# Optimization experiments

Measured on AMD Instinct MI355X. Metric: run time of the kernel, lower is better.

Reference implementation:

```python
import jax, jax.numpy as jnp
import numpy as np

EPS_OT = 0.1        # args.model.ot_reg
N_ITERS = 5         # args.model.ot_transport
COS_EPS = 1e-8      # torch F.cosine_similarity eps
L2_EPS = 1e-12      # torch F.normalize eps
LN_EPS = 1e-5       # nn.LayerNorm default eps
IN_DIM, HID = 768, 256


def setup_inputs() -> dict:
    key = jax.random.key(0)
    ks = jax.random.split(key, 8)
    Ba, Bb, Sa, Sb = 48, 48, 96, 96
    s_in = 1.0 / np.sqrt(IN_DIM)
    return {
        "batch_a": jax.random.normal(ks[0], (Ba, Sa, IN_DIM), jnp.float32),
        "batch_b": jax.random.normal(ks[1], (Bb, Sb, IN_DIM), jnp.float32),
        "Wq": jax.random.normal(ks[2], (IN_DIM, HID), jnp.float32) * s_in,
        "bq": jnp.zeros((HID,), jnp.float32),
        "Wk": jax.random.normal(ks[3], (IN_DIM, HID), jnp.float32) * s_in,
        "bk": jnp.zeros((HID,), jnp.float32),
        "Wv": jax.random.normal(ks[4], (IN_DIM, HID), jnp.float32) * s_in,
        "bv": jnp.zeros((HID,), jnp.float32),
        "ln_g": jnp.ones((HID,), jnp.float32),
        "ln_b": jnp.zeros((HID,), jnp.float32),
    }


def _layernorm(x, g, b):
    mu = jnp.mean(x, axis=-1, keepdims=True)
    var = jnp.var(x, axis=-1, keepdims=True)
    return (x - mu) * jax.lax.rsqrt(var + LN_EPS) * g + b


def _sinkhorn(C):
    # multiplicative Sinkhorn on kernel exp(C/eps); row/col renormalization
    T = jnp.exp(C / EPS_OT)  # [Ba,Bb,Sa,Sb]
    def body(_, T):
        T = T / jnp.sum(T, axis=-1, keepdims=True)
        T = T / jnp.sum(T, axis=-2, keepdims=True)
        return T
    return jax.lax.fori_loop(0, N_ITERS, body, T)


def reference(batch_a, batch_b, Wq, bq, Wk, bk, Wv, bv, ln_g, ln_b):
    q = batch_a @ Wq + bq          # [Ba,Sa,H]
    k = batch_b @ Wk + bk          # [Bb,Sb,H]
    v = batch_b @ Wv + bv          # [Bb,Sb,H]

    # cosine similarity across batches: [Ba,Bb,Sa,Sb]
    qn = q / jnp.maximum(jnp.linalg.norm(q, axis=-1, keepdims=True), COS_EPS)
    kn = k / jnp.maximum(jnp.linalg.norm(k, axis=-1, keepdims=True), COS_EPS)
    C = jnp.einsum('aid,bjd->abij', qn, kn)

    T = jax.lax.stop_gradient(_sinkhorn(C))  # C.detach() in source
    # F.normalize(dim=-1): L2 over last dim
    T = T / jnp.maximum(jnp.linalg.norm(T, axis=-1, keepdims=True), L2_EPS)
    # dropout p=0.0 -> identity (eval)

    attended = jnp.einsum('abij,bjd->abid', T, v) + q[:, None]  # [Ba,Bb,Sa,H]
    return _layernorm(attended, ln_g, ln_b)
```

## Files before the change

### kernel.cpp

```cpp
#include <hip/hip_runtime.h>
#include <hip/hip_bf16.h>

typedef __attribute__((ext_vector_type(4))) float f32x4;
typedef __attribute__((ext_vector_type(8))) short bf16x8;
typedef __attribute__((ext_vector_type(4))) short s16x4;

#define BA 48
#define BB 48
#define SS 96
#define DIN 768
#define HH 256

static __device__ __forceinline__ short f2bf(float f) {
    __hip_bfloat16 h = __float2bfloat16(f);
    return *reinterpret_cast<short*>(&h);
}

static __device__ __forceinline__ f32x4 mfma16(bf16x8 a, bf16x8 b, f32x4 c) {
    return __builtin_amdgcn_mfma_f32_16x16x32_bf16(a, b, c, 0, 0, 0);
}

__global__ __launch_bounds__(256) void prep_kernel(
    const float* __restrict__ Xa, const float* __restrict__ Xb,
    const float* __restrict__ Wq, const float* __restrict__ Wk,
    const float* __restrict__ Wv,
    short* __restrict__ xa, short* __restrict__ xb, short* __restrict__ wt) {
    __shared__ float tile[64][65];
    int bx = blockIdx.x;
    if (bx < 3456) {
        size_t i = (size_t)bx * 256 + threadIdx.x;
        const float* src;
        short* dst;
        size_t off;
        if (i < 442368) { src = Xa; dst = xa; off = i * 8; }
        else            { src = Xb; dst = xb; off = (i - 442368) * 8; }
        f32x4 a = *reinterpret_cast<const f32x4*>(src + off);
        f32x4 b = *reinterpret_cast<const f32x4*>(src + off + 4);
        bf16x8 o;
        o[0] = f2bf(a[0]); o[1] = f2bf(a[1]); o[2] = f2bf(a[2]); o[3] = f2bf(a[3]);
        o[4] = f2bf(b[0]); o[5] = f2bf(b[1]); o[6] = f2bf(b[2]); o[7] = f2bf(b[3]);
        *reinterpret_cast<bf16x8*>(dst + off) = o;
    } else {
        int tt = bx - 3456;
        int k0 = (tt % 12) * 64;
        int n0 = ((tt / 12) % 4) * 64;
        int mat = tt / 48;
        const float* W = (mat == 0) ? Wq : (mat == 1) ? Wk : Wv;
        int t = threadIdx.x;
#pragma unroll
        for (int j = 0; j < 16; ++j) {
            int kk = j * 4 + (t >> 6);
            int nn = t & 63;
            tile[kk][nn] = W[(size_t)(k0 + kk) * HH + n0 + nn];
        }
        __syncthreads();
#pragma unroll
        for (int j = 0; j < 4; ++j) {
            int nn = j * 16 + (t >> 4);
            int kk = (t & 15) * 4;
            s16x4 pk;
#pragma unroll
            for (int i = 0; i < 4; ++i) pk[i] = f2bf(tile[kk + i][nn]);
            *reinterpret_cast<s16x4*>(&wt[(size_t)(mat * HH + n0 + nn) * DIN + k0 + kk]) = pk;
        }
    }
}

__global__ __launch_bounds__(384) void qkv_kernel(
    const short* __restrict__ xa, const short* __restrict__ xb,
    const float* __restrict__ bq, const float* __restrict__ bk, const float* __restrict__ bv,
    const short* __restrict__ wt,
    float* __restrict__ q_ws, float* __restrict__ k_ws, short* __restrict__ vt_ws) {
    __shared__ short vtile[32][104];

    int bb = blockIdx.x;
    int mat = blockIdx.y;
    int c0 = blockIdx.z * 32;
    int tid = threadIdx.x;
    int wave = tid >> 6, lane = tid & 63;
    int c = lane & 15, g = lane >> 4;

    const short* X = ((mat == 0) ? xa : xb) + (size_t)bb * SS * DIN;
    const short* Wt = wt + (size_t)mat * HH * DIN;
    const float* bias = (mat == 0) ? bq : (mat == 1) ? bk : bv;

    const f32x4 z4 = {0.f, 0.f, 0.f, 0.f};
    f32x4 acc[2];
    acc[0] = z4; acc[1] = z4;

    const short* ap = X + (16 * wave + c) * DIN + g * 8;
    const short* bp = Wt + (c0 + c) * DIN + g * 8;
    for (int kk = 0; kk < DIN; kk += 32) {
        bf16x8 af = *reinterpret_cast<const bf16x8*>(ap + kk);
#pragma unroll
        for (int n = 0; n < 2; ++n) {
            bf16x8 bf = *reinterpret_cast<const bf16x8*>(bp + n * 16 * DIN + kk);
            acc[n] = mfma16(af, bf, acc[n]);
        }
    }
#pragma unroll
    for (int n = 0; n < 2; ++n) {
        float bv_ = bias[c0 + n * 16 + c];
#pragma unroll
        for (int r = 0; r < 4; ++r) acc[n][r] += bv_;
    }

    if (mat < 2) {
        float* dst = (mat == 0) ? q_ws : k_ws;
#pragma unroll
        for (int n = 0; n < 2; ++n)
#pragma unroll
            for (int r = 0; r < 4; ++r)
                dst[(bb * SS + 16 * wave + 4 * g + r) * HH + c0 + n * 16 + c] = acc[n][r];
    } else {
#pragma unroll
        for (int n = 0; n < 2; ++n)
#pragma unroll
            for (int r = 0; r < 4; ++r)
                vtile[n * 16 + c][16 * wave + 4 * g + r] = f2bf(acc[n][r]);
        __syncthreads();
        {
            int t = tid;
            int d = t / 12, ch = t % 12;
            bf16x8 pk = *reinterpret_cast<const bf16x8*>(&vtile[d][ch * 8]);
            *reinterpret_cast<bf16x8*>(vt_ws + ((size_t)(bb * HH) + c0 + d) * SS + ch * 8) = pk;
        }
    }
}

__global__ __launch_bounds__(256) void norm_kernel(
    const float* __restrict__ q_ws, const float* __restrict__ k_ws,
    short* __restrict__ qn_ws, short* __restrict__ kn_ws) {
    int row = blockIdx.x * 4 + (threadIdx.x >> 6);
    int lane = threadIdx.x & 63;
    int isq = (row < 4608);
    const float* src = isq ? q_ws : k_ws;
    short* dst = isq ? qn_ws : kn_ws;
    int r = isq ? row : row - 4608;

    f32x4 v = *reinterpret_cast<const f32x4*>(src + (size_t)r * HH + lane * 4);
    float s = v[0] * v[0] + v[1] * v[1] + v[2] * v[2] + v[3] * v[3];
#pragma unroll
    for (int m = 1; m < 64; m <<= 1) s += __shfl_xor(s, m);
    float inv = 1.0f / fmaxf(sqrtf(s), 1e-8f);
    s16x4 o;
#pragma unroll
    for (int j = 0; j < 4; ++j) o[j] = f2bf(v[j] * inv);
    *reinterpret_cast<s16x4*>(dst + (size_t)r * HH + lane * 4) = o;
}

__global__ __launch_bounds__(256, 2) void sink_kernel(
    const short* __restrict__ qn_ws, const short* __restrict__ kn_ws,
    short* __restrict__ t_ws, int a_off) {
    int wave = threadIdx.x >> 6, lane = threadIdx.x & 63;
    int c = lane & 15, g = lane >> 4;
    int b = blockIdx.x * 4 + wave;
    int al = blockIdx.y;
    int a = al + a_off;

    const short* qbase = qn_ws + (size_t)(a * SS) * HH + c * HH + g * 8;
    const short* kbase = kn_ws + (size_t)(b * SS) * HH + c * HH + g * 8;

    const f32x4 z4 = {0.f, 0.f, 0.f, 0.f};
    f32x4 K[6][6];
#pragma unroll
    for (int ti = 0; ti < 6; ++ti)
#pragma unroll
        for (int tj = 0; tj < 6; ++tj) K[ti][tj] = z4;

#pragma unroll
    for (int kk = 0; kk < 8; ++kk) {
        bf16x8 qf[6];
#pragma unroll
        for (int ti = 0; ti < 6; ++ti)
            qf[ti] = *reinterpret_cast<const bf16x8*>(qbase + ti * 16 * HH + kk * 32);
#pragma unroll
        for (int tj = 0; tj < 6; ++tj) {
            bf16x8 kf = *reinterpret_cast<const bf16x8*>(kbase + tj * 16 * HH + kk * 32);
#pragma unroll
            for (int ti = 0; ti < 6; ++ti)
                K[ti][tj] = mfma16(kf, qf[ti], K[ti][tj]);
        }
    }

#pragma unroll
    for (int ti = 0; ti < 6; ++ti)
#pragma unroll
        for (int tj = 0; tj < 6; ++tj)
#pragma unroll
            for (int r = 0; r < 4; ++r)
                K[ti][tj][r] = exp2f(K[ti][tj][r] * 14.4269504088896341f);

    f32x4 v[6];
#pragma unroll
    for (int tj = 0; tj < 6; ++tj) v[tj] = (f32x4){1.f, 1.f, 1.f, 1.f};
    float u[6];

#pragma unroll 1
    for (int it = 0; it < 5; ++it) {
#pragma unroll
        for (int ti = 0; ti < 6; ++ti) {
            f32x4 p0 = K[ti][0] * v[0] + K[ti][1] * v[1];
            f32x4 p1 = K[ti][2] * v[2] + K[ti][3] * v[3];
            f32x4 p2 = K[ti][4] * v[4] + K[ti][5] * v[5];
            f32x4 p = (p0 + p1) + p2;
            float rs = (p[0] + p[1]) + (p[2] + p[3]);
            rs += __shfl_xor(rs, 16);
            rs += __shfl_xor(rs, 32);
            u[ti] = 1.0f / rs;
        }
#pragma unroll
        for (int tj = 0; tj < 6; ++tj) {
            f32x4 c0 = K[0][tj] * u[0] + K[1][tj] * u[1];
            f32x4 c1 = K[2][tj] * u[2] + K[3][tj] * u[3];
            f32x4 c2 = K[4][tj] * u[4] + K[5][tj] * u[5];
            f32x4 cs = (c0 + c1) + c2;
#pragma unroll
            for (int m = 1; m < 16; m <<= 1)
#pragma unroll
                for (int r = 0; r < 4; ++r) cs[r] += __shfl_xor(cs[r], m);
#pragma unroll
            for (int r = 0; r < 4; ++r) v[tj][r] = 1.0f / cs[r];
        }
    }

    short* tp = t_ws + (size_t)(al * BB + b) * SS * SS;
#pragma unroll
    for (int ti = 0; ti < 6; ++ti) {
        f32x4 w[6];
#pragma unroll
        for (int tj = 0; tj < 6; ++tj) w[tj] = K[ti][tj] * v[tj];
        f32x4 q0 = w[0] * w[0] + w[1] * w[1];
        f32x4 q1 = w[2] * w[2] + w[3] * w[3];
        f32x4 q2 = w[4] * w[4] + w[5] * w[5];
        f32x4 qq = (q0 + q1) + q2;
        float ss = (qq[0] + qq[1]) + (qq[2] + qq[3]);
        ss += __shfl_xor(ss, 16);
        ss += __shfl_xor(ss, 32);
        float linv = 1.0f / fmaxf(sqrtf(ss), 1e-12f);
#pragma unroll
        for (int tj = 0; tj < 6; ++tj) {
            s16x4 pk;
#pragma unroll
            for (int r = 0; r < 4; ++r) pk[r] = f2bf(w[tj][r] * linv);
            *reinterpret_cast<s16x4*>(tp + (16 * ti + c) * SS + 16 * tj + 4 * g) = pk;
        }
    }
}

__global__ __launch_bounds__(512) void pv_kernel(
    const short* __restrict__ t_ws, const short* __restrict__ vt_ws,
    const float* __restrict__ q_ws,
    const float* __restrict__ ln_g, const float* __restrict__ ln_b,
    float* __restrict__ out, int a_off) {
    __shared__ float wstats[8][2][SS];

    int b = blockIdx.x, al = blockIdx.y;
    int a = al + a_off;
    int tid = threadIdx.x;
    int w = tid >> 6, lane = tid & 63;
    int c = lane & 15, g = lane >> 4;
    int d0 = w * 32;

    const f32x4 z4 = {0.f, 0.f, 0.f, 0.f};
    f32x4 acc[2][6];
#pragma unroll
    for (int dt = 0; dt < 2; ++dt)
#pragma unroll
        for (int ti = 0; ti < 6; ++ti) acc[dt][ti] = z4;

    const short* vp = vt_ws + ((size_t)(b * HH) + d0 + c) * SS + g * 8;
    const short* tp = t_ws + ((size_t)(al * BB + b)) * SS * SS + c * SS + g * 8;
#pragma unroll
    for (int ks = 0; ks < 3; ++ks) {
        bf16x8 af0 = *reinterpret_cast<const bf16x8*>(vp + ks * 32);
        bf16x8 af1 = *reinterpret_cast<const bf16x8*>(vp + 16 * SS + ks * 32);
#pragma unroll
        for (int ti = 0; ti < 6; ++ti) {
            bf16x8 bf = *reinterpret_cast<const bf16x8*>(tp + ti * 16 * SS + ks * 32);
            acc[0][ti] = mfma16(af0, bf, acc[0][ti]);
            acc[1][ti] = mfma16(af1, bf, acc[1][ti]);
        }
    }

    const float* qa = q_ws + (size_t)a * SS * HH;
#pragma unroll
    for (int ti = 0; ti < 6; ++ti) {
        int i = 16 * ti + c;
        f32x4 q0 = *reinterpret_cast<const f32x4*>(qa + (size_t)i * HH + d0 + 4 * g);
        f32x4 q1 = *reinterpret_cast<const f32x4*>(qa + (size_t)i * HH + d0 + 16 + 4 * g);
        f32x4 x0 = acc[0][ti] + q0;
        f32x4 x1 = acc[1][ti] + q1;
        acc[0][ti] = x0;
        acc[1][ti] = x1;
        f32x4 sv = x0 + x1;
        f32x4 qv = x0 * x0 + x1 * x1;
        float l1 = (sv[0] + sv[1]) + (sv[2] + sv[3]);
        float l2 = (qv[0] + qv[1]) + (qv[2] + qv[3]);
        l1 += __shfl_xor(l1, 16);
        l1 += __shfl_xor(l1, 32);
        l2 += __shfl_xor(l2, 16);
        l2 += __shfl_xor(l2, 32);
        if (g == 0) {
            wstats[w][0][i] = l1;
            wstats[w][1][i] = l2;
        }
    }
    __syncthreads();

    f32x4 g4[2], b4[2];
#pragma unroll
    for (int dt = 0; dt < 2; ++dt) {
        g4[dt] = *reinterpret_cast<const f32x4*>(ln_g + d0 + dt * 16 + 4 * g);
        b4[dt] = *reinterpret_cast<const f32x4*>(ln_b + d0 + dt * 16 + 4 * g);
    }

    float* ob = out + ((size_t)(a * BB + b)) * SS * HH;
#pragma unroll
    for (int ti = 0; ti < 6; ++ti) {
        int i = 16 * ti + c;
        float t1 = ((wstats[0][0][i] + wstats[1][0][i]) + (wstats[2][0][i] + wstats[3][0][i])) +
                   ((wstats[4][0][i] + wstats[5][0][i]) + (wstats[6][0][i] + wstats[7][0][i]));
        float t2 = ((wstats[0][1][i] + wstats[1][1][i]) + (wstats[2][1][i] + wstats[3][1][i])) +
                   ((wstats[4][1][i] + wstats[5][1][i]) + (wstats[6][1][i] + wstats[7][1][i]));
        float mean = t1 * (1.0f / 256.0f);
        float var = t2 * (1.0f / 256.0f) - mean * mean;
        float inv = rsqrtf(var + 1e-5f);
#pragma unroll
        for (int dt = 0; dt < 2; ++dt) {
            f32x4 x = acc[dt][ti];
            f32x4 o;
#pragma unroll
            for (int r = 0; r < 4; ++r)
                o[r] = (x[r] - mean) * inv * g4[dt][r] + b4[dt][r];
            *reinterpret_cast<f32x4*>(ob + (size_t)i * HH + d0 + dt * 16 + 4 * g) = o;
        }
    }
}

extern "C" void kernel_launch(void* const* d_in, const int* in_sizes, int n_in,
                              void* d_out, int out_size, void* d_ws, size_t ws_size,
                              hipStream_t stream) {
    const float* Xa = (const float*)d_in[0];
    const float* Xb = (const float*)d_in[1];
    const float* Wq = (const float*)d_in[2];
    const float* bq = (const float*)d_in[3];
    const float* Wk = (const float*)d_in[4];
    const float* bk = (const float*)d_in[5];
    const float* Wv = (const float*)d_in[6];
    const float* bv = (const float*)d_in[7];
    const float* ln_g = (const float*)d_in[8];
    const float* ln_b = (const float*)d_in[9];
    float* out = (float*)d_out;

    char* ws = (char*)d_ws;
    short* wt    = (short*)(ws);
    short* xa_bf = (short*)(ws + 1179648);
    short* xb_bf = (short*)(ws + 8257536);
    float* q_ws  = (float*)(ws + 15335424);
    float* k_ws  = (float*)(ws + 20054016);
    short* qn_ws = (short*)(ws + 24772608);
    short* kn_ws = (short*)(ws + 27131904);
    short* vt_ws = (short*)(ws + 29491200);

    const size_t t_full = (size_t)BA * BB * SS * SS * 2;
    size_t t_off = 31850496;
    size_t avail = (ws_size > t_off) ? ws_size - t_off : 0;
    int nch;
    if (avail >= t_full) nch = 1;
    else if (avail >= t_full / 2) nch = 2;
    else if (avail >= t_full / 4) nch = 4;
    else { nch = 4; t_off = 0; }
    short* t_ws = (short*)(ws + t_off);
    int apc = BA / nch;

    prep_kernel<<<dim3(3600), dim3(256), 0, stream>>>(Xa, Xb, Wq, Wk, Wv,
                                                      xa_bf, xb_bf, wt);
    qkv_kernel<<<dim3(BA, 3, 8), dim3(384), 0, stream>>>(xa_bf, xb_bf, bq, bk, bv, wt,
                                                         q_ws, k_ws, vt_ws);
    norm_kernel<<<dim3(2304), dim3(256), 0, stream>>>(q_ws, k_ws, qn_ws, kn_ws);
    for (int ch = 0; ch < nch; ++ch) {
        sink_kernel<<<dim3(12, apc), dim3(256), 0, stream>>>(qn_ws, kn_ws, t_ws, ch * apc);
        pv_kernel<<<dim3(BB, apc), dim3(512), 0, stream>>>(t_ws, vt_ws, q_ws,
                                                           ln_g, ln_b, out, ch * apc);
    }
}
```

Baseline: 238.3 us.

## Fuse L2 row normalization into QKV projection kernel, drop norm kernel

Q and K projection blocks now compute all 256 output columns per row, so each block can apply the bias and do the row L2 normalization in registers and write bf16 qn/kn directly. The separate norm kernel, its launch, and the fp32 k_ws round trip are removed. V projection keeps the old 32-column split. The trade-off is far fewer, heavier Q/K blocks (96 instead of 768) that each hold 16 accumulators, which lowers parallelism in that stage and uses uncoalesced scalar stores.

```diff
diff --git a/kernel.cpp b/kernel.cpp
--- a/kernel.cpp
+++ b/kernel.cpp
@@ -66,53 +66,98 @@
     }
 }
 
-__global__ __launch_bounds__(384) void qkv_kernel(
+__global__ __launch_bounds__(384) void qkvn_kernel(
     const short* __restrict__ xa, const short* __restrict__ xb,
     const float* __restrict__ bq, const float* __restrict__ bk, const float* __restrict__ bv,
     const short* __restrict__ wt,
-    float* __restrict__ q_ws, float* __restrict__ k_ws, short* __restrict__ vt_ws) {
+    float* __restrict__ q_ws, short* __restrict__ qn_ws,
+    short* __restrict__ kn_ws, short* __restrict__ vt_ws) {
     __shared__ short vtile[32][104];
 
     int bb = blockIdx.x;
-    int mat = blockIdx.y;
-    int c0 = blockIdx.z * 32;
+    int y = blockIdx.y;
     int tid = threadIdx.x;
     int wave = tid >> 6, lane = tid & 63;
     int c = lane & 15, g = lane >> 4;
 
-    const short* X = ((mat == 0) ? xa : xb) + (size_t)bb * SS * DIN;
-    const short* Wt = wt + (size_t)mat * HH * DIN;
-    const float* bias = (mat == 0) ? bq : (mat == 1) ? bk : bv;
-
     const f32x4 z4 = {0.f, 0.f, 0.f, 0.f};
-    f32x4 acc[2];
-    acc[0] = z4; acc[1] = z4;
-
-    const short* ap = X + (16 * wave + c) * DIN + g * 8;
-    const short* bp = Wt + (c0 + c) * DIN + g * 8;
-    for (int kk = 0; kk < DIN; kk += 32) {
-        bf16x8 af = *reinterpret_cast<const bf16x8*>(ap + kk);
+
+    if (y < 2) {
+        int mat = y;
+        const short* X = ((mat == 0) ? xa : xb) + (size_t)bb * SS * DIN;
+        const short* Wt = wt + (size_t)mat * HH * DIN;
+        const float* bias = (mat == 0) ? bq : bk;
+
+        f32x4 acc[16];
+#pragma unroll
+        for (int n = 0; n < 16; ++n) acc[n] = z4;
+
+        const short* ap = X + (16 * wave + c) * DIN + g * 8;
+        const short* bp = Wt + c * DIN + g * 8;
+        for (int kk = 0; kk < DIN; kk += 32) {
+            bf16x8 af = *reinterpret_cast<const bf16x8*>(ap + kk);
+#pragma unroll
+            for (int n = 0; n < 16; ++n) {
+                bf16x8 bf = *reinterpret_cast<const bf16x8*>(bp + n * 16 * DIN + kk);
+                acc[n] = mfma16(af, bf, acc[n]);
+            }
+        }
+#pragma unroll
+        for (int n = 0; n < 16; ++n) {
+            float bv_ = bias[n * 16 + c];
+#pragma unroll
+            for (int r = 0; r < 4; ++r) acc[n][r] += bv_;
+        }
+
+        float s2[4] = {0.f, 0.f, 0.f, 0.f};
+#pragma unroll
+        for (int n = 0; n < 16; ++n)
+#pragma unroll
+            for (int r = 0; r < 4; ++r) s2[r] += acc[n][r] * acc[n][r];
+#pragma unroll
+        for (int m = 1; m < 16; m <<= 1)
+#pragma unroll
+            for (int r = 0; r < 4; ++r) s2[r] += __shfl_xor(s2[r], m);
+        float inv[4];
+#pragma unroll
+        for (int r = 0; r < 4; ++r) inv[r] = 1.0f / fmaxf(sqrtf(s2[r]), 1e-8f);
+
+        short* qn = (mat == 0) ? qn_ws : kn_ws;
+#pragma unroll
+        for (int n = 0; n < 16; ++n) {
+#pragma unroll
+            for (int r = 0; r < 4; ++r) {
+                int row = bb * SS + 16 * wave + 4 * g + r;
+                int col = n * 16 + c;
+                if (mat == 0) q_ws[(size_t)row * HH + col] = acc[n][r];
+                qn[(size_t)row * HH + col] = f2bf(acc[n][r] * inv[r]);
+            }
+        }
+    } else {
+        int c0 = (y - 2) * 32;
+        const short* X = xb + (size_t)bb * SS * DIN;
+        const short* Wt = wt + (size_t)2 * HH * DIN;
+
+        f32x4 acc[2];
+        acc[0] = z4; acc[1] = z4;
+
+        const short* ap = X + (16 * wave + c) * DIN + g * 8;
+        const short* bp = Wt + (c0 + c) * DIN + g * 8;
+        for (int kk = 0; kk < DIN; kk += 32) {
+            bf16x8 af = *reinterpret_cast<const bf16x8*>(ap + kk);
+#pragma unroll
+            for (int n = 0; n < 2; ++n) {
+                bf16x8 bf = *reinterpret_cast<const bf16x8*>(bp + n * 16 * DIN + kk);
+                acc[n] = mfma16(af, bf, acc[n]);
+            }
+        }
 #pragma unroll
         for (int n = 0; n < 2; ++n) {
-            bf16x8 bf = *reinterpret_cast<const bf16x8*>(bp + n * 16 * DIN + kk);
-            acc[n] = mfma16(af, bf, acc[n]);
-        }
-    }
-#pragma unroll
-    for (int n = 0; n < 2; ++n) {
-        float bv_ = bias[c0 + n * 16 + c];
-#pragma unroll
-        for (int r = 0; r < 4; ++r) acc[n][r] += bv_;
-    }
-
-    if (mat < 2) {
-        float* dst = (mat == 0) ? q_ws : k_ws;
-#pragma unroll
-        for (int n = 0; n < 2; ++n)
-#pragma unroll
-            for (int r = 0; r < 4; ++r)
-                dst[(bb * SS + 16 * wave + 4 * g + r) * HH + c0 + n * 16 + c] = acc[n][r];
-    } else {
+            float bv_ = bv[c0 + n * 16 + c];
+#pragma unroll
+            for (int r = 0; r < 4; ++r) acc[n][r] += bv_;
+        }
+
 #pragma unroll
         for (int n = 0; n < 2; ++n)
 #pragma unroll
@@ -126,27 +171,6 @@
             *reinterpret_cast<bf16x8*>(vt_ws + ((size_t)(bb * HH) + c0 + d) * SS + ch * 8) = pk;
         }
     }
-}
-
-__global__ __launch_bounds__(256) void norm_kernel(
-    const float* __restrict__ q_ws, const float* __restrict__ k_ws,
-    short* __restrict__ qn_ws, short* __restrict__ kn_ws) {
-    int row = blockIdx.x * 4 + (threadIdx.x >> 6);
-    int lane = threadIdx.x & 63;
-    int isq = (row < 4608);
-    const float* src = isq ? q_ws : k_ws;
-    short* dst = isq ? qn_ws : kn_ws;
-    int r = isq ? row : row - 4608;
-
-    f32x4 v = *reinterpret_cast<const f32x4*>(src + (size_t)r * HH + lane * 4);
-    float s = v[0] * v[0] + v[1] * v[1] + v[2] * v[2] + v[3] * v[3];
-#pragma unroll
-    for (int m = 1; m < 64; m <<= 1) s += __shfl_xor(s, m);
-    float inv = 1.0f / fmaxf(sqrtf(s), 1e-8f);
-    s16x4 o;
-#pragma unroll
-    for (int j = 0; j < 4; ++j) o[j] = f2bf(v[j] * inv);
-    *reinterpret_cast<s16x4*>(dst + (size_t)r * HH + lane * 4) = o;
 }
 
 __global__ __launch_bounds__(256, 2) void sink_kernel(
@@ -358,13 +382,12 @@
     short* xa_bf = (short*)(ws + 1179648);
     short* xb_bf = (short*)(ws + 8257536);
     float* q_ws  = (float*)(ws + 15335424);
-    float* k_ws  = (float*)(ws + 20054016);
-    short* qn_ws = (short*)(ws + 24772608);
-    short* kn_ws = (short*)(ws + 27131904);
-    short* vt_ws = (short*)(ws + 29491200);
+    short* qn_ws = (short*)(ws + 20054016);
+    short* kn_ws = (short*)(ws + 22413312);
+    short* vt_ws = (short*)(ws + 24772608);
 
     const size_t t_full = (size_t)BA * BB * SS * SS * 2;
-    size_t t_off = 31850496;
+    size_t t_off = 27131904;
     size_t avail = (ws_size > t_off) ? ws_size - t_off : 0;
     int nch;
     if (avail >= t_full) nch = 1;
@@ -376,9 +399,8 @@
 
     prep_kernel<<<dim3(3600), dim3(256), 0, stream>>>(Xa, Xb, Wq, Wk, Wv,
                                                       xa_bf, xb_bf, wt);
-    qkv_kernel<<<dim3(BA, 3, 8), dim3(384), 0, stream>>>(xa_bf, xb_bf, bq, bk, bv, wt,
-                                                         q_ws, k_ws, vt_ws);
-    norm_kernel<<<dim3(2304), dim3(256), 0, stream>>>(q_ws, k_ws, qn_ws, kn_ws);
+    qkvn_kernel<<<dim3(BA, 10), dim3(384), 0, stream>>>(xa_bf, xb_bf, bq, bk, bv, wt,
+                                                        q_ws, qn_ws, kn_ws, vt_ws);
     for (int ch = 0; ch < nch; ++ch) {
         sink_kernel<<<dim3(12, apc), dim3(256), 0, stream>>>(qn_ws, kn_ws, t_ws, ch * apc);
         pv_kernel<<<dim3(BB, apc), dim3(512), 0, stream>>>(t_ws, vt_ws, q_ws,
```

New measurement: 279.4 us. +17.3%, slower.
